# Optimization experiments

Measured on AMD Instinct MI355X. Metric: run time of the kernel, lower is better.

## Reference

```python
import jax, jax.numpy as jnp
import numpy as np
import math

B, S, H = 4, 2048, 1024
NE, NC, CD, OD = 4, 16, 64, 128  # num_experiments, num_exp_codes, exp_code_dim, outcome_dim
TAU, TEMP, EPS = 0.5, 0.07, 1e-5


def gelu(x):
    return jax.nn.gelu(x, approximate=False)


def layer_norm(x, g, b):
    m = x.mean(-1, keepdims=True)
    v = ((x - m) ** 2).mean(-1, keepdims=True)
    return (x - m) * jax.lax.rsqrt(v + EPS) * g + b


def setup_inputs() -> dict:
    key = jax.random.key(0)
    ks = jax.random.split(key, 24)
    lin = lambda k, i, o: jax.random.normal(k, (i, o), jnp.float32) * 0.02
    u = jax.random.uniform(ks[1], (B, NE, NC), minval=1e-6, maxval=1.0 - 1e-6)
    d = {
        "hidden_states": jax.random.normal(ks[0], (B, S, H), jnp.float32),
        "attention_mask": jnp.ones((B, S), jnp.int32),
        "gumbel_noise": -jnp.log(-jnp.log(u)),
        # context_pooler: Linear(H,H) + LayerNorm
        "cp_w": lin(ks[2], H, H), "cp_b": jnp.zeros(H), "cp_ln_g": jnp.ones(H), "cp_ln_b": jnp.zeros(H),
        # eph: Linear(H,H), Linear(H, NE*NC)
        "eph_w1": lin(ks[3], H, H), "eph_b1": jnp.zeros(H),
        "eph_w2": lin(ks[4], H, NE * NC), "eph_b2": jnp.zeros(NE * NC),
        "codebook": jax.random.normal(ks[5], (NC, CD), jnp.float32) * 0.02,
        # world_kernel: Linear(H+CD, 2H), Linear(2H, OD)
        "wk_w1": lin(ks[6], H + CD, 2 * H), "wk_b1": jnp.zeros(2 * H),
        "wk_w2": lin(ks[7], 2 * H, OD), "wk_b2": jnp.zeros(OD),
        "tp_w": lin(ks[8], H, OD),  # target_proj, no bias
        # film_proj: Linear(OD, 2H) + GELU
        "film_w": lin(ks[9], OD, 2 * H), "film_b": jnp.zeros(2 * H),
        "q_w": lin(ks[10], H, H), "q_b": jnp.zeros(H),
        "k_w": lin(ks[11], H, H), "k_b": jnp.zeros(H),
        "v_w": lin(ks[12], H, H), "v_b": jnp.zeros(H),
        "o_w": lin(ks[13], H, H), "o_b": jnp.zeros(H),
        "int_w": lin(ks[14], H, 4 * H), "int_b": jnp.zeros(4 * H),
        "out_w": lin(ks[15], 4 * H, H), "out_b": jnp.zeros(H),
        "ln_g": jnp.ones(H), "ln_b": jnp.zeros(H),
    }
    return d


def reference(hidden_states, attention_mask, gumbel_noise,
              cp_w, cp_b, cp_ln_g, cp_ln_b,
              eph_w1, eph_b1, eph_w2, eph_b2, codebook,
              wk_w1, wk_b1, wk_w2, wk_b2, tp_w, film_w, film_b,
              q_w, q_b, k_w, k_b, v_w, v_b, o_w, o_b,
              int_w, int_b, out_w, out_b, ln_g, ln_b):
    mask = attention_mask.astype(hidden_states.dtype)  # [B,S]
    # --- context pooling ---
    denom = mask.sum(1, keepdims=True) + 1e-8
    pooled = (hidden_states * mask[:, :, None]).sum(1) / denom  # [B,H]
    h_ctx = layer_norm(gelu(pooled @ cp_w + cp_b), cp_ln_g, cp_ln_b)
    # --- experiment proposal (gumbel-softmax, hard, tau=0.5) ---
    z_raw = gelu(h_ctx @ eph_w1 + eph_b1) @ eph_w2 + eph_b2
    z_logits = z_raw.reshape(B, NE, NC)
    y_soft = jax.nn.softmax((z_logits + gumbel_noise) / TAU, axis=-1)
    y_hard = jax.nn.one_hot(jnp.argmax(y_soft, -1), NC, dtype=y_soft.dtype)
    z_soft = y_hard - jax.lax.stop_gradient(y_soft) + y_soft  # straight-through
    z_codes = z_soft @ codebook  # [B,NE,CD]
    # --- world kernel ---
    h_rep = jnp.broadcast_to(h_ctx[:, None, :], (B, NE, H))
    h_wk = jnp.concatenate([h_rep, z_codes], -1)  # [B,NE,H+CD]
    outcome = gelu(h_wk @ wk_w1 + wk_b1) @ wk_w2 + wk_b2  # [B,NE,OD]
    # --- info gain (labels/plan_vector None branch) ---
    tv = h_ctx @ tp_w
    tv = tv / jnp.linalg.norm(tv, axis=-1, keepdims=True).clip(1e-12)
    on = outcome / jnp.linalg.norm(outcome, axis=-1, keepdims=True).clip(1e-12)
    info_gain = jnp.sum(on * tv[:, None, :], -1) / TEMP  # [B,NE]
    idx = jnp.argmax(info_gain, -1)  # [B]
    chosen = jnp.take_along_axis(outcome, idx[:, None, None], axis=1)[:, 0]  # [B,OD]
    # --- FiLM ---
    gb = gelu(chosen @ film_w + film_b)  # [B,2H]
    gamma, beta = gb[:, :H], gb[:, H:]
    fused = gamma[:, None, :] * hidden_states + beta[:, None, :]  # [B,S,H]
    # --- single-head attention ---
    q = fused @ q_w + q_b
    k = fused @ k_w + k_b
    v = fused @ v_w + v_b
    scores = jnp.einsum('bqd,bkd->bqk', q, k) / math.sqrt(H)
    scores = jnp.where(attention_mask[:, None, :] == 0, -jnp.inf, scores)
    attn = jax.nn.softmax(scores, axis=-1)
    attn_out = jnp.einsum('bqk,bkd->bqd', attn, v) @ o_w + o_b
    # --- FFN + residual + LN ---
    ff = gelu((attn_out + fused) @ int_w + int_b) @ out_w + out_b
    return layer_norm(ff + fused, ln_g, ln_b)
```

## Files before the change

kernel.cpp:

```cpp
#include <hip/hip_runtime.h>
#include <math.h>

#define DEVI __device__ __forceinline__

typedef unsigned short u16;
typedef __attribute__((ext_vector_type(4))) float f32x4;
typedef __attribute__((ext_vector_type(8))) short s16x8;
typedef __attribute__((ext_vector_type(4))) short s16x4;

constexpr int Bc = 4, Sc = 2048, Hc = 1024;
constexpr int NEc = 4, NCc = 16, CDc = 64, ODc = 128;
constexpr float TAUc = 0.5f, TEMPc = 0.07f, EPSc = 1e-5f;

DEVI float gelu_f(float x) { return 0.5f * x * (1.0f + erff(x * 0.7071067811865476f)); }

DEVI float bf2f(u16 u) { union { unsigned int i; float f; } v; v.i = ((unsigned int)u) << 16; return v.f; }
DEVI u16 f2bf(float f) {
  union { float f; unsigned int i; } v; v.f = f;
  unsigned int u = v.i;
  unsigned int r = (u + 0x7fffu + ((u >> 16) & 1u)) >> 16;
  return (u16)r;
}

DEVI float wred_sum(float v) {
  #pragma unroll
  for (int o = 32; o > 0; o >>= 1) v += __shfl_down(v, o);
  return v;
}
DEVI float wred_max(float v) {
  #pragma unroll
  for (int o = 32; o > 0; o >>= 1) v = fmaxf(v, __shfl_down(v, o));
  return v;
}

DEVI void gload16(const void* g, void* l) {
  __builtin_amdgcn_global_load_lds((const __attribute__((address_space(1))) void*)g,
                                   (__attribute__((address_space(3))) void*)l, 16, 0, 0);
}

template<int EPI>
__global__ __launch_bounds__(256, 3) void gemm_bt(
    const u16* __restrict__ A, long sAz, int lda,
    const u16* __restrict__ Bt, long sBz, int ldb,
    u16* __restrict__ C, long sCz, int ldc,
    const float* __restrict__ bias,
    const u16* __restrict__ resid, long sRz,
    float scale, int M, int N, int K)
{
  const int bz = blockIdx.z;
  A += (long)bz * sAz; Bt += (long)bz * sBz; C += (long)bz * sCz;
  if (EPI & 4) resid += (long)bz * sRz;

  int bid = blockIdx.x;
  const int nwg = gridDim.x;
  if ((nwg & 7) == 0) bid = ((bid & 7) * (nwg >> 3)) + (bid >> 3);

  const int nTn = N >> 7;
  const int tm = bid / nTn, tn = bid % nTn;
  const int tid = threadIdx.x;
  const int wid = tid >> 6, lane = tid & 63;
  const int wr = wid >> 1, wc = wid & 1;
  const int l15 = lane & 15, l4 = lane >> 4;

  __shared__ u16 smem[16384];
  u16* As = smem;
  u16* Bs = smem + 8192;

  f32x4 acc[4][4];
  #pragma unroll
  for (int i = 0; i < 4; ++i)
    #pragma unroll
    for (int j = 0; j < 4; ++j) acc[i][j] = f32x4{0.f, 0.f, 0.f, 0.f};

  const int srow8 = lane >> 3;
  const int scol = (((lane & 7) ^ srow8) << 3);
  const u16* aS = A + (long)(tm * 128 + (wid << 5) + srow8) * lda + scol;
  const u16* bS = Bt + (long)(tn * 128 + (wid << 5) + srow8) * ldb + scol;
  u16* aD = &As[wid * 2048];
  u16* bD = &Bs[wid * 2048];

  const int x7 = l15 & 7;
  const int cx0 = ((l4 ^ x7) << 3);
  const int cx1 = (((l4 + 4) ^ x7) << 3);

  for (int k0 = 0; k0 < K; k0 += 64) {
    #pragma unroll
    for (int L = 0; L < 4; ++L) {
      gload16(aS + (long)(L * 8) * lda, aD + L * 512);
      gload16(bS + (long)(L * 8) * ldb, bD + L * 512);
    }
    __syncthreads();
    #pragma unroll
    for (int ks = 0; ks < 2; ++ks) {
      const int cx = ks ? cx1 : cx0;
      s16x8 af[4], bfr[4];
      #pragma unroll
      for (int i = 0; i < 4; ++i)
        af[i] = *(const s16x8*)&As[((wr << 6) + (i << 4) + l15) * 64 + cx];
      #pragma unroll
      for (int j = 0; j < 4; ++j)
        bfr[j] = *(const s16x8*)&Bs[((wc << 6) + (j << 4) + l15) * 64 + cx];
      #pragma unroll
      for (int i = 0; i < 4; ++i)
        #pragma unroll
        for (int j = 0; j < 4; ++j)
          acc[i][j] = __builtin_amdgcn_mfma_f32_16x16x32_bf16(af[i], bfr[j], acc[i][j], 0, 0, 0);
    }
    __syncthreads();
    aS += 64; bS += 64;
  }

  if (!(EPI & 8)) {
    u16 (*Cs)[128] = (u16(*)[128])smem;
    #pragma unroll
    for (int p = 0; p < 2; ++p) {
      if (wr == p) {
        #pragma unroll
        for (int j = 0; j < 4; ++j) {
          const int c = (wc << 6) + (j << 4) + l15;
          const float bv = (EPI & 1) ? bias[tn * 128 + c] : 0.f;
          #pragma unroll
          for (int i = 0; i < 4; ++i) {
            const int lr = (i << 4) + (l4 << 2);
            #pragma unroll
            for (int r = 0; r < 4; ++r) {
              float v = acc[i][j][r] * scale + bv;
              if (EPI & 2) v = gelu_f(v);
              Cs[lr + r][c] = f2bf(v);
            }
          }
        }
      }
      __syncthreads();
      #pragma unroll
      for (int it = 0; it < 4; ++it) {
        const int row = (tid >> 4) + (it << 4);
        const int chunk = tid & 15;
        const long Gr = tm * 128 + (p << 6) + row;
        const int col0 = tn * 128 + (chunk << 3);
        s16x8 cv = *(s16x8*)&Cs[row][chunk << 3];
        if (EPI & 4) {
          const s16x8 rv = *(const s16x8*)&resid[Gr * ldc + col0];
          #pragma unroll
          for (int e = 0; e < 8; ++e)
            cv[e] = (short)f2bf(bf2f((u16)cv[e]) + bf2f((u16)rv[e]));
        }
        *(s16x8*)&C[Gr * ldc + col0] = cv;
      }
      if (p == 0) __syncthreads();
    }
  } else {
    u16 (*Ct)[136] = (u16(*)[136])smem;
    #pragma unroll
    for (int p = 0; p < 2; ++p) {
      if (wc == p) {
        #pragma unroll
        for (int j = 0; j < 4; ++j) {
          const int lc = (j << 4) + l15;
          const float bv = (EPI & 1) ? bias[tn * 128 + (p << 6) + lc] : 0.f;
          #pragma unroll
          for (int i = 0; i < 4; ++i) {
            const int row_lo = (wr << 6) + (i << 4) + (l4 << 2);
            s16x4 pk;
            #pragma unroll
            for (int r = 0; r < 4; ++r) {
              float v = acc[i][j][r] * scale + bv;
              if (EPI & 2) v = gelu_f(v);
              pk[r] = (short)f2bf(v);
            }
            *(s16x4*)&Ct[lc][row_lo] = pk;
          }
        }
      }
      __syncthreads();
      #pragma unroll
      for (int it = 0; it < 4; ++it) {
        const int lc = (tid >> 4) + (it << 4);
        const int chunk = tid & 15;
        const long Gc = tn * 128 + (p << 6) + lc;
        const int col0 = tm * 128 + (chunk << 3);
        s16x8 cv = *(s16x8*)&Ct[lc][chunk << 3];
        *(s16x8*)&C[Gc * ldc + col0] = cv;
      }
      if (p == 0) __syncthreads();
    }
  }
}

__global__ void transpose_w_k(const float* __restrict__ in, u16* __restrict__ out, int K, int N) {
  __shared__ float t[32][33];
  const int n0 = blockIdx.x << 5, k0 = blockIdx.y << 5;
  const int tx = threadIdx.x, ty = threadIdx.y;
  #pragma unroll
  for (int i = 0; i < 32; i += 8)
    t[ty + i][tx] = in[(long)(k0 + ty + i) * N + n0 + tx];
  __syncthreads();
  #pragma unroll
  for (int i = 0; i < 32; i += 8)
    out[(long)(n0 + ty + i) * K + k0 + tx] = f2bf(t[tx][ty + i]);
}

__global__ void transpose_w4_k(const float* __restrict__ w0, const float* __restrict__ w1,
                               const float* __restrict__ w2, const float* __restrict__ w3,
                               u16* __restrict__ o0, u16* __restrict__ o1,
                               u16* __restrict__ o2, u16* __restrict__ o3) {
  const int z = blockIdx.z;
  const float* in = (z == 0) ? w0 : (z == 1) ? w1 : (z == 2) ? w2 : w3;
  u16* out = (z == 0) ? o0 : (z == 1) ? o1 : (z == 2) ? o2 : o3;
  __shared__ float t[32][33];
  const int n0 = blockIdx.x << 5, k0 = blockIdx.y << 5;
  const int tx = threadIdx.x, ty = threadIdx.y;
  #pragma unroll
  for (int i = 0; i < 32; i += 8)
    t[ty + i][tx] = in[(long)(k0 + ty + i) * Hc + n0 + tx];
  __syncthreads();
  #pragma unroll
  for (int i = 0; i < 32; i += 8)
    out[(long)(n0 + ty + i) * Hc + k0 + tx] = f2bf(t[tx][ty + i]);
}

__global__ void concat_bias_k(const float* __restrict__ a, const float* __restrict__ b,
                              float* __restrict__ o) {
  const int i = (blockIdx.x << 8) + threadIdx.x;
  o[i] = (i < Hc) ? a[i] : b[i - Hc];
}

__global__ void pool_partial_k(const float* __restrict__ hs, const int* __restrict__ mask,
                               float* __restrict__ part) {
  const int h = (blockIdx.x << 8) + threadIdx.x;
  const int c = blockIdx.y, b = blockIdx.z;
  const int s0 = c * (Sc / 16);
  float acc = 0.f;
  for (int i = 0; i < Sc / 16; ++i) {
    const int s = s0 + i;
    acc += hs[((long)b * Sc + s) * Hc + h] * (float)mask[b * Sc + s];
  }
  part[((b << 4) + c) * Hc + h] = acc;
}

__global__ void pool_final_k(const float* __restrict__ part, const int* __restrict__ mask,
                             float* __restrict__ pooled) {
  const int b = blockIdx.x;
  __shared__ float red[4];
  __shared__ float denom_s;
  float d = 0.f;
  for (int i = threadIdx.x; i < Sc; i += 256) d += (float)mask[b * Sc + i];
  d = wred_sum(d);
  if ((threadIdx.x & 63) == 0) red[threadIdx.x >> 6] = d;
  __syncthreads();
  if (threadIdx.x == 0) denom_s = red[0] + red[1] + red[2] + red[3] + 1e-8f;
  __syncthreads();
  const float inv = 1.f / denom_s;
  for (int h = threadIdx.x; h < Hc; h += 256) {
    float s = 0.f;
    #pragma unroll
    for (int c = 0; c < 16; ++c) s += part[((b << 4) + c) * Hc + h];
    pooled[b * Hc + h] = s * inv;
  }
}

template<int R>
__global__ void mrow_part_k(const float* __restrict__ in, const float* __restrict__ W,
                            float* __restrict__ part, int K, int N) {
  const int t = threadIdx.x;
  const int jj = t & 31;
  const int j = (blockIdx.x << 5) + jj;
  const int ks = t >> 5;
  const int nchunk = gridDim.y;
  const int Kc = K / (nchunk << 3);
  const int k0 = ((blockIdx.y << 3) + ks) * Kc;
  float acc[R];
  #pragma unroll
  for (int r = 0; r < R; ++r) acc[r] = 0.f;
  for (int k = k0; k < k0 + Kc; ++k) {
    const float wv = W[(long)k * N + j];
    #pragma unroll
    for (int r = 0; r < R; ++r) acc[r] = fmaf(in[r * K + k], wv, acc[r]);
  }
  __shared__ float sm[8][R][32];
  #pragma unroll
  for (int r = 0; r < R; ++r) sm[ks][r][jj] = acc[r];
  __syncthreads();
  for (int idx = t; idx < R * 32; idx += 256) {
    const int r = idx >> 5, j2 = idx & 31;
    float s = 0.f;
    #pragma unroll
    for (int q = 0; q < 8; ++q) s += sm[q][r][j2];
    part[(long)(blockIdx.y * R + r) * N + (blockIdx.x << 5) + j2] = s;
  }
}

template<bool GELU>
__global__ void mrow_reduce_k(const float* __restrict__ part, const float* __restrict__ bias,
                              float* __restrict__ out, int N, int R, int nchunk) {
  const int idx = (blockIdx.x << 8) + threadIdx.x;
  if (idx >= R * N) return;
  const int r = idx / N, j = idx - r * N;
  float s = 0.f;
  for (int c = 0; c < nchunk; ++c) s += part[(long)(c * R + r) * N + j];
  if (bias) s += bias[j];
  if (GELU) s = gelu_f(s);
  out[(long)r * N + j] = s;
}

__global__ void ln_rows_k(float* __restrict__ x, const float* __restrict__ g,
                          const float* __restrict__ b) {
  const long base = (long)blockIdx.x * Hc;
  __shared__ float red[4];
  float v[4]; float s = 0.f;
  #pragma unroll
  for (int i = 0; i < 4; ++i) { v[i] = x[base + threadIdx.x + (i << 8)]; s += v[i]; }
  s = wred_sum(s);
  if ((threadIdx.x & 63) == 0) red[threadIdx.x >> 6] = s;
  __syncthreads();
  const float mean = (red[0] + red[1] + red[2] + red[3]) * (1.f / Hc);
  float q = 0.f;
  #pragma unroll
  for (int i = 0; i < 4; ++i) { const float d2 = v[i] - mean; q += d2 * d2; }
  __syncthreads();
  q = wred_sum(q);
  if ((threadIdx.x & 63) == 0) red[threadIdx.x >> 6] = q;
  __syncthreads();
  const float var = (red[0] + red[1] + red[2] + red[3]) * (1.f / Hc);
  const float inv = rsqrtf(var + EPSc);
  #pragma unroll
  for (int i = 0; i < 4; ++i) {
    const int col = threadIdx.x + (i << 8);
    x[base + col] = (v[i] - mean) * inv * g[col] + b[col];
  }
}

__global__ void gumbel_k(const float* __restrict__ z, const float* __restrict__ gn,
                         const float* __restrict__ cb, float* __restrict__ zcodes) {
  const int b = blockIdx.x, t = threadIdx.x;
  if (t >= NEc) return;
  const float* zp = z + b * (NEc * NCc) + t * NCc;
  const float* gp = gn + (b * NEc + t) * NCc;
  int best = 0; float bv = -3.4e38f;
  for (int c2 = 0; c2 < NCc; ++c2) {
    const float val = (zp[c2] + gp[c2]) * (1.f / TAUc);
    if (val > bv) { bv = val; best = c2; }
  }
  for (int d2 = 0; d2 < CDc; ++d2)
    zcodes[(b * NEc + t) * CDc + d2] = cb[best * CDc + d2];
}

__global__ void build_hwk_k(const float* __restrict__ hctx, const float* __restrict__ zcodes,
                            float* __restrict__ hwk) {
  const int r = blockIdx.x;
  const int b = r >> 2;
  for (int i = threadIdx.x; i < Hc + CDc; i += 256)
    hwk[r * (Hc + CDc) + i] = (i < Hc) ? hctx[b * Hc + i] : zcodes[r * CDc + (i - Hc)];
}

__global__ void select_k(const float* __restrict__ tv, const float* __restrict__ outc,
                         float* __restrict__ chosen) {
  const int b = blockIdx.x, t = threadIdx.x;
  __shared__ float red[2];
  __shared__ float ig[NEc];
  __shared__ int bestIdx;
  const float x = tv[b * ODc + t];
  float ss = wred_sum(x * x);
  if ((t & 63) == 0) red[t >> 6] = ss;
  __syncthreads();
  float nrm = fmaxf(sqrtf(red[0] + red[1]), 1e-12f);
  const float tvn = x / nrm;
  __syncthreads();
  for (int ne = 0; ne < NEc; ++ne) {
    const float o = outc[(b * NEc + ne) * ODc + t];
    float a = wred_sum(o * o);
    float d2 = wred_sum(o * tvn);
    if ((t & 63) == 0) red[t >> 6] = a;
    __syncthreads();
    const float no = sqrtf(red[0] + red[1]);
    __syncthreads();
    if ((t & 63) == 0) red[t >> 6] = d2;
    __syncthreads();
    const float dd = red[0] + red[1];
    if (t == 0) ig[ne] = dd / fmaxf(no, 1e-12f) * (1.f / TEMPc);
    __syncthreads();
  }
  if (t == 0) {
    int bi = 0; float bvv = ig[0];
    for (int ne = 1; ne < NEc; ++ne) if (ig[ne] > bvv) { bvv = ig[ne]; bi = ne; }
    bestIdx = bi;
  }
  __syncthreads();
  chosen[b * ODc + t] = outc[(b * NEc + bestIdx) * ODc + t];
}

__global__ void fuse_k(const float* __restrict__ hs, const float* __restrict__ gb,
                       u16* __restrict__ fused) {
  const long i = (((long)blockIdx.x << 8) + threadIdx.x) << 2;
  const int h = (int)(i & (Hc - 1));
  const int b = (int)(i >> 21);
  const float4 xv = *(const float4*)(hs + i);
  const float* gp = gb + b * 2048;
  s16x4 pk = { (short)f2bf(fmaf(gp[h + 0], xv.x, gp[Hc + h + 0])),
               (short)f2bf(fmaf(gp[h + 1], xv.y, gp[Hc + h + 1])),
               (short)f2bf(fmaf(gp[h + 2], xv.z, gp[Hc + h + 2])),
               (short)f2bf(fmaf(gp[h + 3], xv.w, gp[Hc + h + 3])) };
  *(s16x4*)(fused + i) = pk;
}

__global__ void softmax_k(u16* __restrict__ sc, const int* __restrict__ mask) {
  const long base = (long)blockIdx.x * Sc;
  const int b = blockIdx.x / Sc;
  const int t = threadIdx.x;
  __shared__ float red[4];
  s16x8 v8 = *(s16x8*)&sc[base + t * 8];
  const int4 m0 = *(const int4*)&mask[b * Sc + t * 8];
  const int4 m1 = *(const int4*)&mask[b * Sc + t * 8 + 4];
  float x[8];
  x[0] = (m0.x == 0) ? -3.0e38f : bf2f((u16)v8[0]);
  x[1] = (m0.y == 0) ? -3.0e38f : bf2f((u16)v8[1]);
  x[2] = (m0.z == 0) ? -3.0e38f : bf2f((u16)v8[2]);
  x[3] = (m0.w == 0) ? -3.0e38f : bf2f((u16)v8[3]);
  x[4] = (m1.x == 0) ? -3.0e38f : bf2f((u16)v8[4]);
  x[5] = (m1.y == 0) ? -3.0e38f : bf2f((u16)v8[5]);
  x[6] = (m1.z == 0) ? -3.0e38f : bf2f((u16)v8[6]);
  x[7] = (m1.w == 0) ? -3.0e38f : bf2f((u16)v8[7]);
  float mx = -3.0e38f;
  #pragma unroll
  for (int i = 0; i < 8; ++i) mx = fmaxf(mx, x[i]);
  mx = wred_max(mx);
  if ((t & 63) == 0) red[t >> 6] = mx;
  __syncthreads();
  mx = fmaxf(fmaxf(red[0], red[1]), fmaxf(red[2], red[3]));
  float sum = 0.f;
  #pragma unroll
  for (int i = 0; i < 8; ++i) { x[i] = __expf(x[i] - mx); sum += x[i]; }
  __syncthreads();
  sum = wred_sum(sum);
  if ((t & 63) == 0) red[t >> 6] = sum;
  __syncthreads();
  const float inv = 1.f / (red[0] + red[1] + red[2] + red[3]);
  s16x8 o8;
  #pragma unroll
  for (int i = 0; i < 8; ++i) o8[i] = (short)f2bf(x[i] * inv);
  *(s16x8*)&sc[base + t * 8] = o8;
}

__global__ void final_ln_k(const u16* __restrict__ ff, const u16* __restrict__ fused,
                           const float* __restrict__ g, const float* __restrict__ b,
                           float* __restrict__ out) {
  const long base = (long)blockIdx.x * Hc;
  __shared__ float red[4];
  float v[4]; float s = 0.f;
  #pragma unroll
  for (int i = 0; i < 4; ++i) {
    const int col = threadIdx.x + (i << 8);
    v[i] = bf2f(ff[base + col]) + bf2f(fused[base + col]);
    s += v[i];
  }
  s = wred_sum(s);
  if ((threadIdx.x & 63) == 0) red[threadIdx.x >> 6] = s;
  __syncthreads();
  const float mean = (red[0] + red[1] + red[2] + red[3]) * (1.f / Hc);
  float q = 0.f;
  #pragma unroll
  for (int i = 0; i < 4; ++i) { const float d2 = v[i] - mean; q += d2 * d2; }
  __syncthreads();
  q = wred_sum(q);
  if ((threadIdx.x & 63) == 0) red[threadIdx.x >> 6] = q;
  __syncthreads();
  const float var = (red[0] + red[1] + red[2] + red[3]) * (1.f / Hc);
  const float inv = rsqrtf(var + EPSc);
  #pragma unroll
  for (int i = 0; i < 4; ++i) {
    const int col = threadIdx.x + (i << 8);
    out[base + col] = (v[i] - mean) * inv * g[col] + b[col];
  }
}

extern "C" void kernel_launch(void* const* d_in, const int* in_sizes, int n_in,
                              void* d_out, int out_size, void* d_ws, size_t ws_size,
                              hipStream_t stream) {
  const float* hs       = (const float*)d_in[0];
  const int*   amask    = (const int*)d_in[1];
  const float* gn       = (const float*)d_in[2];
  const float* cp_w     = (const float*)d_in[3];
  const float* cp_b     = (const float*)d_in[4];
  const float* cp_ln_g  = (const float*)d_in[5];
  const float* cp_ln_b  = (const float*)d_in[6];
  const float* eph_w1   = (const float*)d_in[7];
  const float* eph_b1   = (const float*)d_in[8];
  const float* eph_w2   = (const float*)d_in[9];
  const float* eph_b2   = (const float*)d_in[10];
  const float* codebook = (const float*)d_in[11];
  const float* wk_w1    = (const float*)d_in[12];
  const float* wk_b1    = (const float*)d_in[13];
  const float* wk_w2    = (const float*)d_in[14];
  const float* wk_b2    = (const float*)d_in[15];
  const float* tp_w     = (const float*)d_in[16];
  const float* film_w   = (const float*)d_in[17];
  const float* film_b   = (const float*)d_in[18];
  const float* q_w      = (const float*)d_in[19];
  const float* q_bias   = (const float*)d_in[20];
  const float* k_w      = (const float*)d_in[21];
  const float* k_bias   = (const float*)d_in[22];
  const float* v_w      = (const float*)d_in[23];
  const float* v_bias   = (const float*)d_in[24];
  const float* o_w      = (const float*)d_in[25];
  const float* o_bias   = (const float*)d_in[26];
  const float* int_w    = (const float*)d_in[27];
  const float* int_b    = (const float*)d_in[28];
  const float* out_w    = (const float*)d_in[29];
  const float* out_b    = (const float*)d_in[30];
  const float* ln_g     = (const float*)d_in[31];
  const float* ln_b     = (const float*)d_in[32];
  float* outp = (float*)d_out;

  char* w = (char*)d_ws;
  auto alloc = [&](size_t bytes) -> char* {
    char* p = w; w += (bytes + 255) & ~(size_t)255; return p;
  };
  float* part    = (float*)alloc((size_t)Bc * 16 * Hc * 4);
  float* pooled  = (float*)alloc((size_t)Bc * Hc * 4);
  float* hctx    = (float*)alloc((size_t)Bc * Hc * 4);
  float* t1      = (float*)alloc((size_t)Bc * Hc * 4);
  float* zlog    = (float*)alloc((size_t)Bc * 64 * 4);
  float* zcodes  = (float*)alloc((size_t)Bc * NEc * CDc * 4);
  float* hwk     = (float*)alloc((size_t)16 * (Hc + CDc) * 4);
  float* wkt1    = (float*)alloc((size_t)16 * 2048 * 4);
  float* outcome = (float*)alloc((size_t)16 * ODc * 4);
  float* tvb     = (float*)alloc((size_t)Bc * ODc * 4);
  float* chosen  = (float*)alloc((size_t)Bc * ODc * 4);
  float* gb      = (float*)alloc((size_t)Bc * 2048 * 4);
  float* lin_part= (float*)alloc((size_t)1024 * 1024);
  float* qk_bias = (float*)alloc((size_t)2048 * 4);
  u16* qT    = (u16*)alloc((size_t)Hc * Hc * 2);
  u16* kT    = (u16*)alloc((size_t)Hc * Hc * 2);
  u16* vTw   = (u16*)alloc((size_t)Hc * Hc * 2);
  u16* oT    = (u16*)alloc((size_t)Hc * Hc * 2);
  u16* intT  = (u16*)alloc((size_t)Hc * 4096 * 2);
  u16* outT  = (u16*)alloc((size_t)Hc * 4096 * 2);
  u16* fused = (u16*)alloc((size_t)8192 * Hc * 2);
  u16* qkact = (u16*)alloc((size_t)8192 * 2048 * 2);
  u16* scores= (u16*)alloc((size_t)Bc * Sc * Sc * 2);
  u16* vTact = (u16*)alloc((size_t)8192 * Hc * 2);
  u16* attn  = (u16*)alloc((size_t)8192 * Hc * 2);
  u16* h1    = (u16*)alloc((size_t)8192 * Hc * 2);
  u16* mid = qkact;
  u16* ffo = attn;

  if ((size_t)(w - (char*)d_ws) > ws_size) return;

  const dim3 tb32(32, 8);
  transpose_w4_k<<<dim3(32, 32, 4), tb32, 0, stream>>>(q_w, k_w, v_w, o_w, qT, kT, vTw, oT);
  transpose_w_k<<<dim3(4096 / 32, Hc / 32), tb32, 0, stream>>>(int_w, intT, Hc, 4096);
  transpose_w_k<<<dim3(Hc / 32, 4096 / 32), tb32, 0, stream>>>(out_w, outT, 4096, Hc);
  concat_bias_k<<<8, 256, 0, stream>>>(q_bias, k_bias, qk_bias);

  pool_partial_k<<<dim3(Hc / 256, 16, Bc), 256, 0, stream>>>(hs, amask, part);
  pool_final_k<<<Bc, 256, 0, stream>>>(part, amask, pooled);

  mrow_part_k<4><<<dim3(32, 8), 256, 0, stream>>>(pooled, cp_w, lin_part, Hc, Hc);
  mrow_reduce_k<true><<<16, 256, 0, stream>>>(lin_part, cp_b, hctx, Hc, 4, 8);
  ln_rows_k<<<Bc, 256, 0, stream>>>(hctx, cp_ln_g, cp_ln_b);
  mrow_part_k<4><<<dim3(32, 8), 256, 0, stream>>>(hctx, eph_w1, lin_part, Hc, Hc);
  mrow_reduce_k<true><<<16, 256, 0, stream>>>(lin_part, eph_b1, t1, Hc, 4, 8);
  mrow_part_k<4><<<dim3(2, 16), 256, 0, stream>>>(t1, eph_w2, lin_part, Hc, 64);
  mrow_reduce_k<false><<<1, 256, 0, stream>>>(lin_part, eph_b2, zlog, 64, 4, 16);
  gumbel_k<<<Bc, 64, 0, stream>>>(zlog, gn, codebook, zcodes);
  build_hwk_k<<<Bc * NEc, 256, 0, stream>>>(hctx, zcodes, hwk);
  mrow_part_k<16><<<dim3(64, 8), 256, 0, stream>>>(hwk, wk_w1, lin_part, Hc + CDc, 2048);
  mrow_reduce_k<true><<<128, 256, 0, stream>>>(lin_part, wk_b1, wkt1, 2048, 16, 8);
  mrow_part_k<16><<<dim3(4, 32), 256, 0, stream>>>(wkt1, wk_w2, lin_part, 2048, ODc);
  mrow_reduce_k<false><<<8, 256, 0, stream>>>(lin_part, wk_b2, outcome, ODc, 16, 32);
  mrow_part_k<4><<<dim3(4, 8), 256, 0, stream>>>(hctx, tp_w, lin_part, Hc, ODc);
  mrow_reduce_k<false><<<2, 256, 0, stream>>>(lin_part, nullptr, tvb, ODc, 4, 8);
  select_k<<<Bc, 128, 0, stream>>>(tvb, outcome, chosen);
  mrow_part_k<4><<<dim3(64, 2), 256, 0, stream>>>(chosen, film_w, lin_part, ODc, 2048);
  mrow_reduce_k<true><<<32, 256, 0, stream>>>(lin_part, film_b, gb, 2048, 4, 2);
  fuse_k<<<8192, 256, 0, stream>>>(hs, gb, fused);

  gemm_bt<1><<<dim3(1024), 256, 0, stream>>>(fused, 0, Hc, qT, 0, Hc, qkact, 0, 2048,
                                             qk_bias, nullptr, 0, 1.f, 8192, 2048, Hc);
  gemm_bt<9><<<dim3(512), 256, 0, stream>>>(fused, 0, Hc, vTw, 0, Hc, vTact, 0, 8192,
                                            v_bias, nullptr, 0, 1.f, 8192, Hc, Hc);
  gemm_bt<0><<<dim3(256, 1, Bc), 256, 0, stream>>>(qkact, (long)Sc * 2048, 2048,
                                                   qkact + 1024, (long)Sc * 2048, 2048,
                                                   scores, (long)Sc * Sc, Sc,
                                                   nullptr, nullptr, 0, 0.03125f, Sc, Sc, Hc);
  softmax_k<<<Bc * Sc, 256, 0, stream>>>(scores, amask);
  gemm_bt<0><<<dim3(128, 1, Bc), 256, 0, stream>>>(scores, (long)Sc * Sc, Sc,
                                                   vTact, (long)Sc, 8192,
                                                   attn, (long)Sc * Hc, Hc,
                                                   nullptr, nullptr, 0, 1.f, Sc, Hc, Sc);
  gemm_bt<5><<<dim3(512), 256, 0, stream>>>(attn, 0, Hc, oT, 0, Hc, h1, 0, Hc,
                                            o_bias, fused, 0, 1.f, 8192, Hc, Hc);
  gemm_bt<3><<<dim3(2048), 256, 0, stream>>>(h1, 0, Hc, intT, 0, Hc, mid, 0, 4096,
                                             int_b, nullptr, 0, 1.f, 8192, 4096, Hc);
  gemm_bt<1><<<dim3(512), 256, 0, stream>>>(mid, 0, 4096, outT, 0, 4096, ffo, 0, Hc,
                                            out_b, nullptr, 0, 1.f, 8192, Hc, 4096);
  final_ln_k<<<Bc * Sc, 256, 0, stream>>>(ffo, fused, ln_g, ln_b, outp);
}
```

Baseline: 492.3 us.

## Fuse weight transposes and small head kernels, add tile-grouped GEMM block swizzle

```diff
diff --git a/kernel.cpp b/kernel.cpp
--- a/kernel.cpp
+++ b/kernel.cpp
@@ -51,12 +51,21 @@
   A += (long)bz * sAz; Bt += (long)bz * sBz; C += (long)bz * sCz;
   if (EPI & 4) resid += (long)bz * sRz;
 
-  int bid = blockIdx.x;
-  const int nwg = gridDim.x;
-  if ((nwg & 7) == 0) bid = ((bid & 7) * (nwg >> 3)) + (bid >> 3);
-
   const int nTn = N >> 7;
-  const int tm = bid / nTn, tn = bid % nTn;
+  int tm, tn;
+  {
+    const int nwg = gridDim.x;
+    int bid = blockIdx.x;
+    if ((nwg & 7) == 0 && ((nwg >> 3) % nTn) == 0) {
+      const int rows = (nwg >> 3) / nTn;
+      const int x = bid & 7, local = bid >> 3;
+      tm = x * rows + (local % rows);
+      tn = local / rows;
+    } else {
+      if ((nwg & 7) == 0) bid = ((bid & 7) * (nwg >> 3)) + (bid >> 3);
+      tm = bid / nTn; tn = bid % nTn;
+    }
+  }
   const int tid = threadIdx.x;
   const int wid = tid >> 6, lane = tid & 63;
   const int wr = wid >> 1, wc = wid & 1;
@@ -187,42 +196,44 @@
   }
 }
 
-__global__ void transpose_w_k(const float* __restrict__ in, u16* __restrict__ out, int K, int N) {
-  __shared__ float t[32][33];
-  const int n0 = blockIdx.x << 5, k0 = blockIdx.y << 5;
-  const int tx = threadIdx.x, ty = threadIdx.y;
+__global__ void mega_transpose_k(
+    const float* __restrict__ q_w, const float* __restrict__ k_w,
+    const float* __restrict__ v_w, const float* __restrict__ o_w,
+    const float* __restrict__ int_w, const float* __restrict__ out_w,
+    const float* __restrict__ q_bias, const float* __restrict__ k_bias,
+    u16* __restrict__ qT, u16* __restrict__ kT, u16* __restrict__ vTw,
+    u16* __restrict__ oT, u16* __restrict__ intT, u16* __restrict__ outT,
+    float* __restrict__ qk_bias)
+{
+  const int id = blockIdx.x;
+  const int t = threadIdx.x, tx = t & 31, ty = t >> 5;
+  if (id >= 12288) {
+    const int i = ((id - 12288) << 8) + t;
+    qk_bias[i] = (i < Hc) ? q_bias[i] : k_bias[i - Hc];
+    return;
+  }
+  const float* in; u16* out; int K, N, bx, by;
+  if (id < 4096) {
+    const int w = id >> 10, r = id & 1023;
+    in  = (w == 0) ? q_w : (w == 1) ? k_w : (w == 2) ? v_w : o_w;
+    out = (w == 0) ? qT  : (w == 1) ? kT  : (w == 2) ? vTw : oT;
+    K = Hc; N = Hc; bx = r & 31; by = r >> 5;
+  } else if (id < 8192) {
+    const int r = id - 4096;
+    in = int_w; out = intT; K = Hc; N = 4096; bx = r & 127; by = r >> 7;
+  } else {
+    const int r = id - 8192;
+    in = out_w; out = outT; K = 4096; N = Hc; bx = r & 31; by = r >> 5;
+  }
+  __shared__ float tb[32][33];
+  const int n0 = bx << 5, k0 = by << 5;
   #pragma unroll
   for (int i = 0; i < 32; i += 8)
-    t[ty + i][tx] = in[(long)(k0 + ty + i) * N + n0 + tx];
+    tb[ty + i][tx] = in[(long)(k0 + ty + i) * N + n0 + tx];
   __syncthreads();
   #pragma unroll
   for (int i = 0; i < 32; i += 8)
-    out[(long)(n0 + ty + i) * K + k0 + tx] = f2bf(t[tx][ty + i]);
-}
-
-__global__ void transpose_w4_k(const float* __restrict__ w0, const float* __restrict__ w1,
-                               const float* __restrict__ w2, const float* __restrict__ w3,
-                               u16* __restrict__ o0, u16* __restrict__ o1,
-                               u16* __restrict__ o2, u16* __restrict__ o3) {
-  const int z = blockIdx.z;
-  const float* in = (z == 0) ? w0 : (z == 1) ? w1 : (z == 2) ? w2 : w3;
-  u16* out = (z == 0) ? o0 : (z == 1) ? o1 : (z == 2) ? o2 : o3;
-  __shared__ float t[32][33];
-  const int n0 = blockIdx.x << 5, k0 = blockIdx.y << 5;
-  const int tx = threadIdx.x, ty = threadIdx.y;
-  #pragma unroll
-  for (int i = 0; i < 32; i += 8)
-    t[ty + i][tx] = in[(long)(k0 + ty + i) * Hc + n0 + tx];
-  __syncthreads();
-  #pragma unroll
-  for (int i = 0; i < 32; i += 8)
-    out[(long)(n0 + ty + i) * Hc + k0 + tx] = f2bf(t[tx][ty + i]);
-}
-
-__global__ void concat_bias_k(const float* __restrict__ a, const float* __restrict__ b,
-                              float* __restrict__ o) {
-  const int i = (blockIdx.x << 8) + threadIdx.x;
-  o[i] = (i < Hc) ? a[i] : b[i - Hc];
+    out[(long)(n0 + ty + i) * K + k0 + tx] = f2bf(tb[tx][ty + i]);
 }
 
 __global__ void pool_partial_k(const float* __restrict__ hs, const int* __restrict__ mask,
@@ -303,15 +314,23 @@
   out[(long)r * N + j] = s;
 }
 
-__global__ void ln_rows_k(float* __restrict__ x, const float* __restrict__ g,
-                          const float* __restrict__ b) {
-  const long base = (long)blockIdx.x * Hc;
+__global__ void reduce_ln_cp_k(const float* __restrict__ part, const float* __restrict__ bias,
+                               const float* __restrict__ g, const float* __restrict__ bb,
+                               float* __restrict__ hctx) {
+  const int b = blockIdx.x, t = threadIdx.x;
   __shared__ float red[4];
   float v[4]; float s = 0.f;
   #pragma unroll
-  for (int i = 0; i < 4; ++i) { v[i] = x[base + threadIdx.x + (i << 8)]; s += v[i]; }
+  for (int i = 0; i < 4; ++i) {
+    const int col = t + (i << 8);
+    float a = bias[col];
+    #pragma unroll
+    for (int c = 0; c < 8; ++c) a += part[(long)((c << 2) + b) * Hc + col];
+    v[i] = gelu_f(a);
+    s += v[i];
+  }
   s = wred_sum(s);
-  if ((threadIdx.x & 63) == 0) red[threadIdx.x >> 6] = s;
+  if ((t & 63) == 0) red[t >> 6] = s;
   __syncthreads();
   const float mean = (red[0] + red[1] + red[2] + red[3]) * (1.f / Hc);
   float q = 0.f;
@@ -319,38 +338,46 @@
   for (int i = 0; i < 4; ++i) { const float d2 = v[i] - mean; q += d2 * d2; }
   __syncthreads();
   q = wred_sum(q);
-  if ((threadIdx.x & 63) == 0) red[threadIdx.x >> 6] = q;
+  if ((t & 63) == 0) red[t >> 6] = q;
   __syncthreads();
   const float var = (red[0] + red[1] + red[2] + red[3]) * (1.f / Hc);
   const float inv = rsqrtf(var + EPSc);
   #pragma unroll
   for (int i = 0; i < 4; ++i) {
-    const int col = threadIdx.x + (i << 8);
-    x[base + col] = (v[i] - mean) * inv * g[col] + b[col];
-  }
-}
-
-__global__ void gumbel_k(const float* __restrict__ z, const float* __restrict__ gn,
-                         const float* __restrict__ cb, float* __restrict__ zcodes) {
-  const int b = blockIdx.x, t = threadIdx.x;
-  if (t >= NEc) return;
-  const float* zp = z + b * (NEc * NCc) + t * NCc;
-  const float* gp = gn + (b * NEc + t) * NCc;
-  int best = 0; float bv = -3.4e38f;
-  for (int c2 = 0; c2 < NCc; ++c2) {
-    const float val = (zp[c2] + gp[c2]) * (1.f / TAUc);
-    if (val > bv) { bv = val; best = c2; }
-  }
-  for (int d2 = 0; d2 < CDc; ++d2)
-    zcodes[(b * NEc + t) * CDc + d2] = cb[best * CDc + d2];
-}
-
-__global__ void build_hwk_k(const float* __restrict__ hctx, const float* __restrict__ zcodes,
-                            float* __restrict__ hwk) {
-  const int r = blockIdx.x;
-  const int b = r >> 2;
-  for (int i = threadIdx.x; i < Hc + CDc; i += 256)
-    hwk[r * (Hc + CDc) + i] = (i < Hc) ? hctx[b * Hc + i] : zcodes[r * CDc + (i - Hc)];
+    const int col = t + (i << 8);
+    hctx[b * Hc + col] = (v[i] - mean) * inv * g[col] + bb[col];
+  }
+}
+
+__global__ void zcode_fused_k(const float* __restrict__ part, const float* __restrict__ bias,
+                              const float* __restrict__ gn, const float* __restrict__ cb,
+                              const float* __restrict__ hctx, float* __restrict__ hwk) {
+  const int t = threadIdx.x;
+  __shared__ float zl[256];
+  __shared__ int best[16];
+  {
+    const int r = t >> 6, j = t & 63;
+    float s = bias[j];
+    #pragma unroll
+    for (int c = 0; c < 16; ++c) s += part[((c << 2) + r) * 64 + j];
+    zl[t] = s;
+  }
+  __syncthreads();
+  if (t < 16) {
+    const int b = t >> 2, e = t & 3;
+    int bi = 0; float bv = -3.4e38f;
+    for (int c = 0; c < NCc; ++c) {
+      const float val = (zl[(b << 6) + (e << 4) + c] + gn[((b << 2) + e) * NCc + c]) * (1.f / TAUc);
+      if (val > bv) { bv = val; bi = c; }
+    }
+    best[t] = bi;
+  }
+  __syncthreads();
+  for (int i = t; i < 16 * 1088; i += 256) {
+    const int r = i / 1088, col = i - r * 1088;
+    const int b = r >> 2;
+    hwk[i] = (col < Hc) ? hctx[b * Hc + col] : cb[best[r] * CDc + (col - Hc)];
+  }
 }
 
 __global__ void select_k(const float* __restrict__ tv, const float* __restrict__ outc,
@@ -519,8 +546,6 @@
   float* pooled  = (float*)alloc((size_t)Bc * Hc * 4);
   float* hctx    = (float*)alloc((size_t)Bc * Hc * 4);
   float* t1      = (float*)alloc((size_t)Bc * Hc * 4);
-  float* zlog    = (float*)alloc((size_t)Bc * 64 * 4);
-  float* zcodes  = (float*)alloc((size_t)Bc * NEc * CDc * 4);
   float* hwk     = (float*)alloc((size_t)16 * (Hc + CDc) * 4);
   float* wkt1    = (float*)alloc((size_t)16 * 2048 * 4);
   float* outcome = (float*)alloc((size_t)16 * ODc * 4);
@@ -546,24 +571,19 @@
 
   if ((size_t)(w - (char*)d_ws) > ws_size) return;
 
-  const dim3 tb32(32, 8);
-  transpose_w4_k<<<dim3(32, 32, 4), tb32, 0, stream>>>(q_w, k_w, v_w, o_w, qT, kT, vTw, oT);
-  transpose_w_k<<<dim3(4096 / 32, Hc / 32), tb32, 0, stream>>>(int_w, intT, Hc, 4096);
-  transpose_w_k<<<dim3(Hc / 32, 4096 / 32), tb32, 0, stream>>>(out_w, outT, 4096, Hc);
-  concat_bias_k<<<8, 256, 0, stream>>>(q_bias, k_bias, qk_bias);
+  mega_transpose_k<<<12296, 256, 0, stream>>>(q_w, k_w, v_w, o_w, int_w, out_w,
+                                              q_bias, k_bias,
+                                              qT, kT, vTw, oT, intT, outT, qk_bias);
 
   pool_partial_k<<<dim3(Hc / 256, 16, Bc), 256, 0, stream>>>(hs, amask, part);
   pool_final_k<<<Bc, 256, 0, stream>>>(part, amask, pooled);
 
   mrow_part_k<4><<<dim3(32, 8), 256, 0, stream>>>(pooled, cp_w, lin_part, Hc, Hc);
-  mrow_reduce_k<true><<<16, 256, 0, stream>>>(lin_part, cp_b, hctx, Hc, 4, 8);
-  ln_rows_k<<<Bc, 256, 0, stream>>>(hctx, cp_ln_g, cp_ln_b);
+  reduce_ln_cp_k<<<Bc, 256, 0, stream>>>(lin_part, cp_b, cp_ln_g, cp_ln_b, hctx);
   mrow_part_k<4><<<dim3(32, 8), 256, 0, stream>>>(hctx, eph_w1, lin_part, Hc, Hc);
   mrow_reduce_k<true><<<16, 256, 0, stream>>>(lin_part, eph_b1, t1, Hc, 4, 8);
   mrow_part_k<4><<<dim3(2, 16), 256, 0, stream>>>(t1, eph_w2, lin_part, Hc, 64);
-  mrow_reduce_k<false><<<1, 256, 0, stream>>>(lin_part, eph_b2, zlog, 64, 4, 16);
-  gumbel_k<<<Bc, 64, 0, stream>>>(zlog, gn, codebook, zcodes);
-  build_hwk_k<<<Bc * NEc, 256, 0, stream>>>(hctx, zcodes, hwk);
+  zcode_fused_k<<<1, 256, 0, stream>>>(lin_part, eph_b2, gn, codebook, hctx, hwk);
   mrow_part_k<16><<<dim3(64, 8), 256, 0, stream>>>(hwk, wk_w1, lin_part, Hc + CDc, 2048);
   mrow_reduce_k<true><<<128, 256, 0, stream>>>(lin_part, wk_b1, wkt1, 2048, 16, 8);
   mrow_part_k<16><<<dim3(4, 32), 256, 0, stream>>>(wkt1, wk_w2, lin_part, 2048, ODc);
```

Result: no change. 495.6 us (+0.7%).
